# Kernel optimization log

Measured on AMD Instinct MI355X. Metric: run time of the kernel, lower is better.

## Reference

```python
import jax, jax.numpy as jnp
import numpy as np

NUM_KNOTS = 10
DEGREE = 3
NUM_BASIS = NUM_KNOTS + DEGREE - 1  # 12
IN_FEATURES = 512
OUT_FEATURES = 512


def _interval_bounds():
    # t = linspace(0,1,num_knots); segment i covers [t[max(0,i-deg+1)], t[min(i+1,K-1)])
    t = np.linspace(0.0, 1.0, NUM_KNOTS, dtype=np.float32)
    idx = np.arange(NUM_BASIS)
    lower = t[np.maximum(0, idx - (DEGREE - 1))]
    upper = t[np.minimum(idx + 1, NUM_KNOTS - 1)]
    return jnp.asarray(lower), jnp.asarray(upper)


def setup_inputs() -> dict:
    key = jax.random.key(0)
    kx, kc = jax.random.split(key)
    x = jax.random.uniform(kx, (8, 2048, IN_FEATURES), dtype=jnp.float32)
    # coeffs for spline (i=out, j=in): torch indexes splines[i*in_features+j]
    coeffs = jax.random.normal(kc, (OUT_FEATURES, IN_FEATURES, NUM_BASIS), dtype=jnp.float32)
    return {"x": x, "coeffs": coeffs}


def reference(x, coeffs):
    lower, upper = _interval_bounds()  # [NUM_BASIS] each
    # piecewise-constant basis masks: [b, s, in, NUM_BASIS]
    xe = x[..., None]
    basis = ((xe >= lower) & (xe < upper)).astype(x.dtype)
    # out[b,s,i] = sum_j sum_k basis[b,s,j,k] * coeffs[i,j,k]
    return jnp.einsum("bsjk,ijk->bsi", basis, coeffs)
```

## Files before the change

### kernel.cpp

```cpp
#include <hip/hip_runtime.h>

#define MTOT 16384
#define NFEAT 512
#define KTOT 4608

typedef float f32x4 __attribute__((ext_vector_type(4)));
typedef short s16x8 __attribute__((ext_vector_type(8)));

__device__ __forceinline__ int div9(int c) { return (c * 7282) >> 16; }

#define GLDS(GP, LP) __builtin_amdgcn_global_load_lds( \
    (const __attribute__((address_space(1))) void*)(GP), \
    (__attribute__((address_space(3))) void*)(LP), 16, 0, 0)

__device__ __forceinline__ s16x8 decode_frag(unsigned code) {
  unsigned nb0 = code & 15u, nb1 = code >> 4;
  unsigned p0 = nb0 - 1u, p1 = nb1 - 1u;
  unsigned long long v0 = (nb0 ? 0x3F80ull : 0ull) << ((p0 & 3u) << 4);
  unsigned long long v1 = (nb1 ? 0x3F80ull : 0ull) << ((p1 & 3u) << 4);
  unsigned long long lo = (p0 < 4u ? v0 : 0ull) | (p1 < 4u ? v1 : 0ull);
  unsigned long long hi = (p0 < 4u ? 0ull : v0) | (p1 < 4u ? 0ull : v1);
  union { unsigned long long q[2]; s16x8 v; } u;
  u.q[0] = lo; u.q[1] = hi;
  return u.v;
}

__global__ __launch_bounds__(256) void prep(const float* __restrict__ x,
                                            const float* __restrict__ coeffs,
                                            unsigned char* __restrict__ codeT,
                                            unsigned short* __restrict__ Bmat) {
  __shared__ unsigned char segt[64][68];
  const int bx = blockIdx.x;
  const int tid = threadIdx.x;
  if (bx < 2048) {
    const int i = bx >> 2, q = bx & 3;
    const float* cb = coeffs + (size_t)i * 6144;
#pragma unroll
    for (int p = 0; p < 5; ++p) {
      int kl = p * 256 + tid;
      if (kl < 1152) {
        int k = q * 1152 + kl;
        int j = div9(k), s = k - j * 9;
        float v = cb[j * 12 + s] + cb[j * 12 + s + 1] + cb[j * 12 + s + 2];
        unsigned u = __float_as_uint(v);
        unsigned rn = (u + 0x7FFFu + ((u >> 16) & 1u)) >> 16;
        Bmat[(size_t)i * KTOT + k] = (unsigned short)rn;
      }
    }
  } else {
    const int bb = bx - 2048;
    const int mt = bb >> 3;
    const int jt = bb & 7;
    const int m0 = mt * 64;
    const float4* x4 = (const float4*)x;
    const float T1 = (float)(1.0/9.0), T2 = (float)(2.0/9.0), T3 = (float)(3.0/9.0),
                T4 = (float)(4.0/9.0), T5 = (float)(5.0/9.0), T6 = (float)(6.0/9.0),
                T7 = (float)(7.0/9.0), T8 = (float)(8.0/9.0);
#pragma unroll
    for (int it = 0; it < 4; ++it) {
      int f = it * 256 + tid;
      int m = f >> 4, jq = f & 15;
      float4 v = x4[(size_t)(m0 + m) * 128 + jt * 16 + jq];
      uchar4 sv;
      { float xv = v.x; sv.x = (unsigned char)((xv>=T1)+(xv>=T2)+(xv>=T3)+(xv>=T4)+(xv>=T5)+(xv>=T6)+(xv>=T7)+(xv>=T8)); }
      { float xv = v.y; sv.y = (unsigned char)((xv>=T1)+(xv>=T2)+(xv>=T3)+(xv>=T4)+(xv>=T5)+(xv>=T6)+(xv>=T7)+(xv>=T8)); }
      { float xv = v.z; sv.z = (unsigned char)((xv>=T1)+(xv>=T2)+(xv>=T3)+(xv>=T4)+(xv>=T5)+(xv>=T6)+(xv>=T7)+(xv>=T8)); }
      { float xv = v.w; sv.w = (unsigned char)((xv>=T1)+(xv>=T2)+(xv>=T3)+(xv>=T4)+(xv>=T5)+(xv>=T6)+(xv>=T7)+(xv>=T8)); }
      *(uchar4*)&segt[m][jq * 4] = sv;
    }
    __syncthreads();
#pragma unroll
    for (int p = 0; p < 5; ++p) {
      int u = p * 256 + tid;
      if (u < 1152) {
        int gl = u >> 4, mq = u & 15;
        int c0 = jt * 576 + gl * 8;
        int j0 = div9(c0), j1 = div9(c0 + 7);
        int j0l = j0 - jt * 64, j1l = j1 - jt * 64;
        uchar4 ob;
        unsigned char* pb = (unsigned char*)&ob;
#pragma unroll
        for (int c = 0; c < 4; ++c) {
          int m = mq * 4 + c;
          int s0 = segt[m][j0l];
          int pos0 = j0 * 9 + s0 - c0;
          unsigned code = (pos0 >= 0 && pos0 < 8) ? (unsigned)(pos0 + 1) : 0u;
          if (j1 != j0) {
            int s1 = segt[m][j1l];
            int pos1 = j1 * 9 + s1 - c0;
            if (pos1 < 8) code |= (unsigned)(pos1 + 1) << 4;
          }
          pb[c] = (unsigned char)code;
        }
        *(uchar4*)(codeT + (size_t)(jt * 72 + gl) * MTOT + m0 + mq * 4) = ob;
      }
    }
  }
}

__global__ __launch_bounds__(256, 2) void kan_gemm(const unsigned char* __restrict__ codeT,
                                                   const unsigned short* __restrict__ Bmat,
                                                   float* __restrict__ out) {
  __shared__ __align__(16) short Blds[2][16 * 512];
  const int tid = threadIdx.x;
  const int lane = tid & 63;
  const int wid = tid >> 6;
  const int lm = lane & 15;
  const int lq = lane >> 4;
  const int bx = blockIdx.x;
  const int rr8 = bx & 7, qq = bx >> 3;
  const int nt = rr8 & 3;
  const int mt = qq * 2 + (rr8 >> 2);
  const int m0 = mt * 128, n0 = nt * 128;
  const int wr = wid;

  const unsigned short* gB0 = Bmat + (size_t)(n0 + (wid * 2 + 0) * 16 + lm) * KTOT + lq * 8;
  const unsigned short* gB1 = Bmat + (size_t)(n0 + (wid * 2 + 1) * 16 + lm) * KTOT + lq * 8;
  const unsigned char* gC0 = codeT + (size_t)lq * MTOT + m0 + wr * 32 + lm;
  const unsigned char* gC1 = codeT + (size_t)(4 + lq) * MTOT + m0 + wr * 32 + lm;

  f32x4 acc[2][8] = {};
  s16x8 afA[4], afB[4];
  unsigned char cr[4];

#define LOAD_CR() do { \
    cr[0] = gC0[0]; cr[1] = gC1[0]; cr[2] = gC0[16]; cr[3] = gC1[16]; \
    gC0 += (size_t)8 * MTOT; gC1 += (size_t)8 * MTOT; } while (0)

#define ISSUE_B(buf) do { \
    short* base = &Blds[buf][0] + wid * 2048; \
    GLDS(gB0,      base);        \
    GLDS(gB0 + 32, base + 512);  \
    GLDS(gB1,      base + 1024); \
    GLDS(gB1 + 32, base + 1536); \
    gB0 += 64; gB1 += 64; } while (0)

#define COMPUTE(AF, buf) do { \
    _Pragma("unroll") \
    for (int ks = 0; ks < 2; ++ks) { \
      s16x8 bf[8]; \
      _Pragma("unroll") \
      for (int ns = 0; ns < 8; ++ns) \
        bf[ns] = *(const s16x8*)&Blds[buf][(ns * 2 + ks) * 512 + lane * 8]; \
      _Pragma("unroll") \
      for (int ms = 0; ms < 2; ++ms) \
        _Pragma("unroll") \
        for (int ns = 0; ns < 8; ++ns) \
          acc[ms][ns] = __builtin_amdgcn_mfma_f32_16x16x32_bf16(AF[ms * 2 + ks], bf[ns], acc[ms][ns], 0, 0, 0); \
    } } while (0)

  LOAD_CR();
  ISSUE_B(0);
#pragma unroll
  for (int f = 0; f < 4; ++f) afA[f] = decode_frag(cr[f]);
  LOAD_CR();
  __syncthreads();

#pragma unroll 1
  for (int kt = 0; kt < 72; kt += 2) {
    ISSUE_B(1);
#pragma unroll
    for (int f = 0; f < 4; ++f) afB[f] = decode_frag(cr[f]);
    if (kt < 70) LOAD_CR();
    COMPUTE(afA, 0);
    __syncthreads();
    if (kt < 70) {
      ISSUE_B(0);
#pragma unroll
      for (int f = 0; f < 4; ++f) afA[f] = decode_frag(cr[f]);
      LOAD_CR();
    }
    COMPUTE(afB, 1);
    __syncthreads();
  }

#pragma unroll
  for (int ms = 0; ms < 2; ++ms) {
#pragma unroll
    for (int ns = 0; ns < 8; ++ns) {
      int tok = m0 + wr * 32 + ms * 16 + lq * 4;
      int col = n0 + ns * 16 + lm;
      float* op = out + (size_t)tok * NFEAT + col;
#pragma unroll
      for (int rg = 0; rg < 4; ++rg) op[(size_t)rg * NFEAT] = acc[ms][ns][rg];
    }
  }
}

extern "C" void kernel_launch(void* const* d_in, const int* in_sizes, int n_in,
                              void* d_out, int out_size, void* d_ws, size_t ws_size,
                              hipStream_t stream) {
  const float* x = (const float*)d_in[0];
  const float* coeffs = (const float*)d_in[1];
  float* out = (float*)d_out;
  unsigned char* codeT = (unsigned char*)d_ws;
  unsigned short* Bmat = (unsigned short*)((char*)d_ws + (size_t)576 * MTOT);

  prep<<<dim3(4096), dim3(256), 0, stream>>>(x, coeffs, codeT, Bmat);
  kan_gemm<<<dim3(512), dim3(256), 0, stream>>>(codeT, Bmat, out);
}
```

Before: 171.0 us.

## Deepen GEMM pipeline to four LDS stages with explicit vmcnt waits

The B-tile LDS buffer grows from a double to a quadruple ring, with three tiles and four code-byte sets kept in flight. __syncthreads is replaced by hand-counted s_waitcnt vmcnt waits plus raw barriers, and MFMA blocks are wrapped in s_setprio. The goal is to hide global-to-LDS latency better and avoid full waits on every barrier. LDS use doubles to 64KB per block, which may cut occupancy below 2 blocks per CU, and the manual vmcnt counts are fragile.

```diff
diff --git a/kernel.cpp b/kernel.cpp
--- a/kernel.cpp
+++ b/kernel.cpp
@@ -101,7 +101,7 @@
 __global__ __launch_bounds__(256, 2) void kan_gemm(const unsigned char* __restrict__ codeT,
                                                    const unsigned short* __restrict__ Bmat,
                                                    float* __restrict__ out) {
-  __shared__ __align__(16) short Blds[2][16 * 512];
+  __shared__ __align__(16) short Blds[4][16 * 512];
   const int tid = threadIdx.x;
   const int lane = tid & 63;
   const int wid = tid >> 6;
@@ -120,59 +120,91 @@
   const unsigned char* gC1 = codeT + (size_t)(4 + lq) * MTOT + m0 + wr * 32 + lm;
 
   f32x4 acc[2][8] = {};
-  s16x8 afA[4], afB[4];
-  unsigned char cr[4];
-
-#define LOAD_CR() do { \
-    cr[0] = gC0[0]; cr[1] = gC1[0]; cr[2] = gC0[16]; cr[3] = gC1[16]; \
+  s16x8 afX[4], afY[4];
+  unsigned char crQ[4][4];
+
+#define CRLOAD(SET) do { \
+    crQ[SET][0] = gC0[0]; crQ[SET][1] = gC1[0]; \
+    crQ[SET][2] = gC0[16]; crQ[SET][3] = gC1[16]; \
     gC0 += (size_t)8 * MTOT; gC1 += (size_t)8 * MTOT; } while (0)
 
-#define ISSUE_B(buf) do { \
-    short* base = &Blds[buf][0] + wid * 2048; \
+#define ISSUE_B(SLOT) do { \
+    short* base = &Blds[SLOT][0] + wid * 2048; \
     GLDS(gB0,      base);        \
     GLDS(gB0 + 32, base + 512);  \
     GLDS(gB1,      base + 1024); \
     GLDS(gB1 + 32, base + 1536); \
     gB0 += 64; gB1 += 64; } while (0)
 
-#define COMPUTE(AF, buf) do { \
+#define DECODE(SET, AF) do { \
+    _Pragma("unroll") \
+    for (int f = 0; f < 4; ++f) AF[f] = decode_frag(crQ[SET][f]); } while (0)
+
+#define COMPUTE(AF, SLOT) do { \
+    __builtin_amdgcn_s_setprio(1); \
     _Pragma("unroll") \
     for (int ks = 0; ks < 2; ++ks) { \
       s16x8 bf[8]; \
       _Pragma("unroll") \
       for (int ns = 0; ns < 8; ++ns) \
-        bf[ns] = *(const s16x8*)&Blds[buf][(ns * 2 + ks) * 512 + lane * 8]; \
+        bf[ns] = *(const s16x8*)&Blds[SLOT][(ns * 2 + ks) * 512 + lane * 8]; \
       _Pragma("unroll") \
       for (int ms = 0; ms < 2; ++ms) \
         _Pragma("unroll") \
         for (int ns = 0; ns < 8; ++ns) \
           acc[ms][ns] = __builtin_amdgcn_mfma_f32_16x16x32_bf16(AF[ms * 2 + ks], bf[ns], acc[ms][ns], 0, 0, 0); \
-    } } while (0)
-
-  LOAD_CR();
-  ISSUE_B(0);
-#pragma unroll
-  for (int f = 0; f < 4; ++f) afA[f] = decode_frag(cr[f]);
-  LOAD_CR();
-  __syncthreads();
+    } \
+    __builtin_amdgcn_s_setprio(0); } while (0)
+
+#define VWAIT(N) asm volatile("s_waitcnt vmcnt(" #N ")" ::: "memory")
+#define FENCE()  asm volatile("" ::: "memory")
+#define BAR()    __builtin_amdgcn_s_barrier()
+
+  CRLOAD(0); FENCE();
+  CRLOAD(1); ISSUE_B(0); FENCE();
+  CRLOAD(2); ISSUE_B(1); FENCE();
+  CRLOAD(3); ISSUE_B(2); FENCE();
+  VWAIT(24);
+  DECODE(0, afX);
 
 #pragma unroll 1
-  for (int kt = 0; kt < 72; kt += 2) {
-    ISSUE_B(1);
-#pragma unroll
-    for (int f = 0; f < 4; ++f) afB[f] = decode_frag(cr[f]);
-    if (kt < 70) LOAD_CR();
-    COMPUTE(afA, 0);
-    __syncthreads();
-    if (kt < 70) {
-      ISSUE_B(0);
-#pragma unroll
-      for (int f = 0; f < 4; ++f) afA[f] = decode_frag(cr[f]);
-      LOAD_CR();
-    }
-    COMPUTE(afB, 1);
-    __syncthreads();
+  for (int k = 0; k < 17; ++k) {
+    VWAIT(16); BAR();
+    CRLOAD(0); ISSUE_B(3);
+    DECODE(1, afY);
+    COMPUTE(afX, 0);
+
+    VWAIT(16); BAR();
+    CRLOAD(1); ISSUE_B(0);
+    DECODE(2, afX);
+    COMPUTE(afY, 1);
+
+    VWAIT(16); BAR();
+    CRLOAD(2); ISSUE_B(1);
+    DECODE(3, afY);
+    COMPUTE(afX, 2);
+
+    VWAIT(16); BAR();
+    CRLOAD(3); ISSUE_B(2);
+    DECODE(0, afX);
+    COMPUTE(afY, 3);
   }
+
+  VWAIT(16); BAR();
+  ISSUE_B(3);
+  DECODE(1, afY);
+  COMPUTE(afX, 0);
+
+  VWAIT(12); BAR();
+  DECODE(2, afX);
+  COMPUTE(afY, 1);
+
+  VWAIT(4); BAR();
+  DECODE(3, afY);
+  COMPUTE(afX, 2);
+
+  VWAIT(0); BAR();
+  COMPUTE(afY, 3);
 
 #pragma unroll
   for (int ms = 0; ms < 2; ++ms) {
@@ -185,6 +217,13 @@
       for (int rg = 0; rg < 4; ++rg) op[(size_t)rg * NFEAT] = acc[ms][ns][rg];
     }
   }
+#undef CRLOAD
+#undef ISSUE_B
+#undef DECODE
+#undef COMPUTE
+#undef VWAIT
+#undef FENCE
+#undef BAR
 }
 
 extern "C" void kernel_launch(void* const* d_in, const int* in_sizes, int n_in,
```

Result: slower. 177.9 us (+4.1%).

## Split K across warp pairs with LDS reduction and smaller M tiles in GEMM

Applied to the files above, without the earlier changes.

The GEMM kernel now uses 64x128 tiles and launches twice as many blocks. Within each block, two warp pairs each handle half of the K dimension and their partial accumulators are combined through LDS at the end. The code layout in prep is changed to interleave tokens so each lane can fetch two codes with one 16-bit load. The main loop uses explicit vmcnt waits, raw barriers and setprio to overlap loads with MFMA, and occupancy is raised to four blocks per CU. In exchange, each block loads B with less reuse across M, and the final reduction adds LDS traffic.

```diff
diff --git a/kernel.cpp b/kernel.cpp
--- a/kernel.cpp
+++ b/kernel.cpp
@@ -81,7 +81,7 @@
         unsigned char* pb = (unsigned char*)&ob;
 #pragma unroll
         for (int c = 0; c < 4; ++c) {
-          int m = mq * 4 + c;
+          int m = mq + c * 16;
           int s0 = segt[m][j0l];
           int pos0 = j0 * 9 + s0 - c0;
           unsigned code = (pos0 >= 0 && pos0 < 8) ? (unsigned)(pos0 + 1) : 0u;
@@ -98,93 +98,110 @@
   }
 }
 
-__global__ __launch_bounds__(256, 2) void kan_gemm(const unsigned char* __restrict__ codeT,
+__global__ __launch_bounds__(256, 4) void kan_gemm(const unsigned char* __restrict__ codeT,
                                                    const unsigned short* __restrict__ Bmat,
                                                    float* __restrict__ out) {
-  __shared__ __align__(16) short Blds[2][16 * 512];
+  __shared__ __align__(16) short Blds[2][2][4096];
   const int tid = threadIdx.x;
   const int lane = tid & 63;
   const int wid = tid >> 6;
+  const int mh = wid & 1;
+  const int kh = wid >> 1;
   const int lm = lane & 15;
   const int lq = lane >> 4;
   const int bx = blockIdx.x;
-  const int rr8 = bx & 7, qq = bx >> 3;
-  const int nt = rr8 & 3;
-  const int mt = qq * 2 + (rr8 >> 2);
-  const int m0 = mt * 128, n0 = nt * 128;
-  const int wr = wid;
-
-  const unsigned short* gB0 = Bmat + (size_t)(n0 + (wid * 2 + 0) * 16 + lm) * KTOT + lq * 8;
-  const unsigned short* gB1 = Bmat + (size_t)(n0 + (wid * 2 + 1) * 16 + lm) * KTOT + lq * 8;
-  const unsigned char* gC0 = codeT + (size_t)lq * MTOT + m0 + wr * 32 + lm;
-  const unsigned char* gC1 = codeT + (size_t)(4 + lq) * MTOT + m0 + wr * 32 + lm;
+  const int mt = bx >> 2;
+  const int nt = bx & 3;
+  const int m0 = mt * 64, n0 = nt * 128;
+
+  const unsigned short* gB0 = Bmat + (size_t)(n0 + (mh * 4 + 0) * 16 + lm) * KTOT + kh * 2304 + lq * 8;
+  const unsigned short* gB1 = Bmat + (size_t)(n0 + (mh * 4 + 1) * 16 + lm) * KTOT + kh * 2304 + lq * 8;
+  const unsigned short* gB2 = Bmat + (size_t)(n0 + (mh * 4 + 2) * 16 + lm) * KTOT + kh * 2304 + lq * 8;
+  const unsigned short* gB3 = Bmat + (size_t)(n0 + (mh * 4 + 3) * 16 + lm) * KTOT + kh * 2304 + lq * 8;
+  const unsigned char* gCp = codeT + (size_t)(kh * 288 + lq) * MTOT + m0 + lm * 4 + mh * 2;
 
   f32x4 acc[2][8] = {};
-  s16x8 afA[4], afB[4];
-  unsigned char cr[4];
-
-#define LOAD_CR() do { \
-    cr[0] = gC0[0]; cr[1] = gC1[0]; cr[2] = gC0[16]; cr[3] = gC1[16]; \
-    gC0 += (size_t)8 * MTOT; gC1 += (size_t)8 * MTOT; } while (0)
-
-#define ISSUE_B(buf) do { \
-    short* base = &Blds[buf][0] + wid * 2048; \
-    GLDS(gB0,      base);        \
-    GLDS(gB0 + 32, base + 512);  \
-    GLDS(gB1,      base + 1024); \
-    GLDS(gB1 + 32, base + 1536); \
-    gB0 += 64; gB1 += 64; } while (0)
-
-#define COMPUTE(AF, buf) do { \
+  s16x8 af[2];
+  unsigned crQ[2];
+
+#define CRLOAD(SET) do { \
+    crQ[SET] = *(const unsigned short*)gCp; gCp += (size_t)4 * MTOT; } while (0)
+
+#define ISSUE_B(SLOT) do { \
+    short* base = &Blds[kh][SLOT][0] + mh * 2048; \
+    GLDS(gB0, base);        GLDS(gB1, base + 512);  \
+    GLDS(gB2, base + 1024); GLDS(gB3, base + 1536); \
+    gB0 += 32; gB1 += 32; gB2 += 32; gB3 += 32; } while (0)
+
+#define DECODE(SET) do { \
+    af[0] = decode_frag(crQ[SET] & 255u); \
+    af[1] = decode_frag((crQ[SET] >> 8) & 255u); } while (0)
+
+#define COMPUTE(SLOT) do { \
+    __builtin_amdgcn_s_setprio(1); \
     _Pragma("unroll") \
-    for (int ks = 0; ks < 2; ++ks) { \
-      s16x8 bf[8]; \
-      _Pragma("unroll") \
-      for (int ns = 0; ns < 8; ++ns) \
-        bf[ns] = *(const s16x8*)&Blds[buf][(ns * 2 + ks) * 512 + lane * 8]; \
-      _Pragma("unroll") \
-      for (int ms = 0; ms < 2; ++ms) \
-        _Pragma("unroll") \
-        for (int ns = 0; ns < 8; ++ns) \
-          acc[ms][ns] = __builtin_amdgcn_mfma_f32_16x16x32_bf16(AF[ms * 2 + ks], bf[ns], acc[ms][ns], 0, 0, 0); \
-    } } while (0)
-
-  LOAD_CR();
-  ISSUE_B(0);
-#pragma unroll
-  for (int f = 0; f < 4; ++f) afA[f] = decode_frag(cr[f]);
-  LOAD_CR();
-  __syncthreads();
+    for (int ns = 0; ns < 8; ++ns) { \
+      s16x8 bf = *(const s16x8*)&Blds[kh][SLOT][ns * 512 + lane * 8]; \
+      acc[0][ns] = __builtin_amdgcn_mfma_f32_16x16x32_bf16(af[0], bf, acc[0][ns], 0, 0, 0); \
+      acc[1][ns] = __builtin_amdgcn_mfma_f32_16x16x32_bf16(af[1], bf, acc[1][ns], 0, 0, 0); \
+    } \
+    __builtin_amdgcn_s_setprio(0); } while (0)
+
+#define VWAIT(N) asm volatile("s_waitcnt vmcnt(" #N ")" ::: "memory")
+#define FENCE()  asm volatile("" ::: "memory")
+#define BAR()    __builtin_amdgcn_s_barrier()
+
+  CRLOAD(0); ISSUE_B(0); FENCE();
+  CRLOAD(1); ISSUE_B(1); FENCE();
 
 #pragma unroll 1
-  for (int kt = 0; kt < 72; kt += 2) {
-    ISSUE_B(1);
-#pragma unroll
-    for (int f = 0; f < 4; ++f) afB[f] = decode_frag(cr[f]);
-    if (kt < 70) LOAD_CR();
-    COMPUTE(afA, 0);
-    __syncthreads();
-    if (kt < 70) {
-      ISSUE_B(0);
-#pragma unroll
-      for (int f = 0; f < 4; ++f) afA[f] = decode_frag(cr[f]);
-      LOAD_CR();
-    }
-    COMPUTE(afB, 1);
-    __syncthreads();
-  }
-
-#pragma unroll
-  for (int ms = 0; ms < 2; ++ms) {
-#pragma unroll
-    for (int ns = 0; ns < 8; ++ns) {
-      int tok = m0 + wr * 32 + ms * 16 + lq * 4;
-      int col = n0 + ns * 16 + lm;
-      float* op = out + (size_t)tok * NFEAT + col;
-#pragma unroll
-      for (int rg = 0; rg < 4; ++rg) op[(size_t)rg * NFEAT] = acc[ms][ns][rg];
-    }
-  }
+  for (int t = 0; t < 70; ++t) {
+    const int set = t & 1;
+    VWAIT(5); BAR();
+    DECODE(set);
+    COMPUTE(set);
+    BAR();
+    CRLOAD(set); ISSUE_B(set);
+  }
+  VWAIT(5); BAR();
+  DECODE(0); COMPUTE(0);
+  BAR();
+  VWAIT(0); BAR();
+  DECODE(1); COMPUTE(1);
+
+  BAR();
+  if (kh == 1) {
+    float* p = (float*)(&Blds[0][0][0]) + (size_t)mh * 4096;
+#pragma unroll
+    for (int ms = 0; ms < 2; ++ms)
+#pragma unroll
+      for (int ns = 0; ns < 8; ++ns)
+#pragma unroll
+        for (int rg = 0; rg < 4; ++rg)
+          p[((ms * 8 + ns) * 4 + rg) * 64 + lane] = acc[ms][ns][rg];
+  }
+  BAR();
+  if (kh == 0) {
+    const float* p = (const float*)(&Blds[0][0][0]) + (size_t)mh * 4096;
+#pragma unroll
+    for (int ms = 0; ms < 2; ++ms)
+#pragma unroll
+      for (int ns = 0; ns < 8; ++ns) {
+        int tok = m0 + mh * 32 + ms * 16 + lq * 4;
+        int col = n0 + ns * 16 + lm;
+        float* op = out + (size_t)tok * NFEAT + col;
+#pragma unroll
+        for (int rg = 0; rg < 4; ++rg)
+          op[(size_t)rg * NFEAT] = acc[ms][ns][rg] + p[((ms * 8 + ns) * 4 + rg) * 64 + lane];
+      }
+  }
+#undef CRLOAD
+#undef ISSUE_B
+#undef DECODE
+#undef COMPUTE
+#undef VWAIT
+#undef FENCE
+#undef BAR
 }
 
 extern "C" void kernel_launch(void* const* d_in, const int* in_sizes, int n_in,
@@ -197,5 +214,5 @@
   unsigned short* Bmat = (unsigned short*)((char*)d_ws + (size_t)576 * MTOT);
 
   prep<<<dim3(4096), dim3(256), 0, stream>>>(x, coeffs, codeT, Bmat);
-  kan_gemm<<<dim3(512), dim3(256), 0, stream>>>(codeT, Bmat, out);
-}
+  kan_gemm<<<dim3(1024), dim3(256), 0, stream>>>(codeT, Bmat, out);
+}
```

New measurement: 255.4 us. +49.4%, slower.
